# Performance work log

Hardware: AMD Instinct MI355X
Metric: run time of the kernel (lower is better)

The kernel has to match this reference:

```python
import jax, jax.numpy as jnp
import numpy as np


def setup_inputs() -> dict:
    key = jax.random.key(0)
    k1, _ = jax.random.split(key)
    N, H, CH, T = 4, 8, 64, 2048
    qkv = jax.random.normal(k1, (N, H * 3 * CH, T), dtype=jnp.float32)
    rescale = jnp.ones((1,), dtype=jnp.float32)
    return {"qkv": qkv, "rescale": rescale, "n_heads": H}


def reference(qkv, rescale, n_heads):
    bs, width, length = qkv.shape
    ch = width // (3 * n_heads)
    # [N, H*3*C, T] -> [N*H, 3*C, T] -> three [N*H, C, T]
    qkv_h = qkv.reshape(bs * n_heads, 3 * ch, length)
    q, k, v = qkv_h[:, :ch], qkv_h[:, ch:2 * ch], qkv_h[:, 2 * ch:]
    scale = 1.0 / jnp.sqrt(jnp.sqrt(jnp.float32(ch)))
    # scores: [B*H, T, S]
    weight = jnp.einsum('bct,bcs->bts', q * scale, k * scale)
    weight = jax.nn.softmax(weight.astype(jnp.float32) * rescale[0], axis=-1).astype(qkv.dtype)
    a = jnp.einsum('bts,bcs->bct', weight, v)  # [B*H, C, T]
    return a.reshape(bs, n_heads * ch, length)
```

## Files before the change

### kernel.cpp

```cpp
#include <hip/hip_runtime.h>
#include <stdint.h>

typedef _Float16 half8 __attribute__((ext_vector_type(8)));
typedef _Float16 half4 __attribute__((ext_vector_type(4)));
typedef __fp16   fp16x2 __attribute__((ext_vector_type(2)));
typedef float    floatx4 __attribute__((ext_vector_type(4)));

#define T_LEN 2048
#define CH 64
#define BH 32
#define QTILE 128
#define LDP 72
#define PTP 72
#define FRAG_BH 131072

__global__ __launch_bounds__(256, 2)
void prep_kernel(const float* __restrict__ qkv, const float* __restrict__ rescale,
                 _Float16* __restrict__ ws)
{
    __shared__ _Float16 Qs[64][LDP];
    __shared__ _Float16 Ks[64][LDP];
    __shared__ _Float16 Vs[64][LDP];

    const int tid  = threadIdx.x;
    const int bh   = blockIdx.y;
    const int tile = blockIdx.x;
    const int x0   = tile * 64;

    const float qscale = 0.125f * 1.4426950408889634f * rescale[0];

    const float* qp = qkv + (size_t)(bh >> 3) * (1536 * T_LEN)
                          + (size_t)(bh & 7) * (192 * T_LEN);
    const float* kp = qp + 64 * T_LEN;
    const float* vp = qp + 128 * T_LEN;

    {
        const int a4 = (tid & 15) * 4;
        const int c4 = (tid >> 4) * 4;
        float4 rq[4], rk[4];
#pragma unroll
        for (int i = 0; i < 4; ++i) {
            rq[i] = *(const float4*)(qp + (size_t)(c4 + i) * T_LEN + x0 + a4);
            rk[i] = *(const float4*)(kp + (size_t)(c4 + i) * T_LEN + x0 + a4);
        }
#pragma unroll
        for (int j = 0; j < 4; ++j) {
            half4 hq, hk;
#pragma unroll
            for (int i = 0; i < 4; ++i) {
                hq[i] = (_Float16)((&rq[i].x)[j] * qscale);
                hk[i] = (_Float16)((&rk[i].x)[j]);
            }
            *(half4*)&Qs[a4 + j][c4] = hq;
            *(half4*)&Ks[a4 + j][c4] = hk;
        }
        const int s4 = (tid & 15) * 4;
        const int cv = tid >> 4;
#pragma unroll
        for (int i = 0; i < 4; ++i) {
            const int c = cv + 16 * i;
            float4 r = *(const float4*)(vp + (size_t)c * T_LEN + x0 + s4);
            half4 h; h[0]=(_Float16)r.x; h[1]=(_Float16)r.y; h[2]=(_Float16)r.z; h[3]=(_Float16)r.w;
            *(half4*)&Vs[c][s4] = h;
        }
    }
    __syncthreads();

    const int lane = tid & 63, wave = tid >> 6;
    const int l15 = lane & 15, quad = lane >> 4;
    _Float16* qf = ws;
    _Float16* kf = ws + (size_t)BH * FRAG_BH;
    _Float16* vf = ws + (size_t)2 * BH * FRAG_BH;

#pragma unroll
    for (int ks = 0; ks < 2; ++ks) {
        half8 hq = *(const half8*)&Qs[wave * 16 + l15][ks * 32 + quad * 8];
        half8 hk = *(const half8*)&Ks[wave * 16 + l15][ks * 32 + quad * 8];
        half8 hv = *(const half8*)&Vs[wave * 16 + l15][ks * 32 + quad * 8];
        const size_t gqk = (((size_t)bh * 128 + tile * 4 + wave) * 2 + ks) * 512 + lane * 8;
        *(half8*)(qf + gqk) = hq;
        *(half8*)(kf + gqk) = hk;
        *(half8*)(vf + (((size_t)bh * 32 + tile) * 8 + wave * 2 + ks) * 512 + lane * 8) = hv;
    }
}

__global__ __launch_bounds__(256, 2)
void attn_kernel(const _Float16* __restrict__ ws, float* __restrict__ out)
{
    __shared__ _Float16 Pt[4][32][PTP];

    const int tid  = threadIdx.x;
    const int wave = tid >> 6;
    const int lane = tid & 63;
    const int l15  = lane & 15;
    const int quad = lane >> 4;

    const int bh = blockIdx.y;
    const int t0 = blockIdx.x * QTILE;

    const _Float16* qf = ws;
    const _Float16* kf = ws + (size_t)BH * FRAG_BH;
    const _Float16* vf = ws + (size_t)2 * BH * FRAG_BH;
    float* op = out + (size_t)bh * (CH * T_LEN);

    const _Float16* kfp = kf + (size_t)bh * FRAG_BH + lane * 8;
    const _Float16* vfp = vf + (size_t)bh * FRAG_BH + lane * 8;

    half8 bq[2][2];
#pragma unroll
    for (int tb = 0; tb < 2; ++tb)
#pragma unroll
        for (int ks = 0; ks < 2; ++ks)
            bq[tb][ks] = *(const half8*)(qf +
                (((size_t)bh * 128 + blockIdx.x * 8 + wave * 2 + tb) * 2 + ks) * 512 + lane * 8);

    const floatx4 fzero = {0.f, 0.f, 0.f, 0.f};
    floatx4 oacc[2][4];
#pragma unroll
    for (int tb = 0; tb < 2; ++tb)
#pragma unroll
        for (int ct = 0; ct < 4; ++ct) oacc[tb][ct] = fzero;
    floatx4 lacc[2] = {fzero, fzero};

    half8 bones;
#pragma unroll
    for (int i = 0; i < 8; ++i) bones[i] = (_Float16)1.0f;

    half8 ak[4][2];
    half8 bv[4][2];
    half8 ap[2][2];

    auto do_qk_exp = [&]() {
        floatx4 sacc[4][2];
#pragma unroll
        for (int mt = 0; mt < 4; ++mt)
#pragma unroll
            for (int tb = 0; tb < 2; ++tb) sacc[mt][tb] = fzero;
#pragma unroll
        for (int mt = 0; mt < 4; ++mt)
#pragma unroll
            for (int tb = 0; tb < 2; ++tb)
#pragma unroll
                for (int ks = 0; ks < 2; ++ks)
                    sacc[mt][tb] = __builtin_amdgcn_mfma_f32_16x16x32_f16(
                        ak[mt][ks], bq[tb][ks], sacc[mt][tb], 0, 0, 0);

#pragma unroll
        for (int mt = 0; mt < 4; ++mt)
#pragma unroll
            for (int tb = 0; tb < 2; ++tb) {
                fp16x2 p01 = __builtin_amdgcn_cvt_pkrtz(
                    __builtin_amdgcn_exp2f(sacc[mt][tb][0]),
                    __builtin_amdgcn_exp2f(sacc[mt][tb][1]));
                fp16x2 p23 = __builtin_amdgcn_cvt_pkrtz(
                    __builtin_amdgcn_exp2f(sacc[mt][tb][2]),
                    __builtin_amdgcn_exp2f(sacc[mt][tb][3]));
                half4 ph;
                ph[0] = (_Float16)p01[0]; ph[1] = (_Float16)p01[1];
                ph[2] = (_Float16)p23[0]; ph[3] = (_Float16)p23[1];
                *(half4*)&Pt[wave][tb * 16 + l15][mt * 16 + quad * 4] = ph;
            }
#pragma unroll
        for (int tb = 0; tb < 2; ++tb)
#pragma unroll
            for (int ks = 0; ks < 2; ++ks)
                ap[tb][ks] = *(const half8*)&Pt[wave][tb * 16 + l15][ks * 32 + quad * 8];
    };

#pragma unroll
    for (int mt = 0; mt < 4; ++mt)
#pragma unroll
        for (int ks = 0; ks < 2; ++ks)
            ak[mt][ks] = *(const half8*)(kfp + (size_t)(mt * 2 + ks) * 512);
#pragma unroll
    for (int ct = 0; ct < 4; ++ct)
#pragma unroll
        for (int ks = 0; ks < 2; ++ks)
            bv[ct][ks] = *(const half8*)(vfp + (size_t)(ct * 2 + ks) * 512);
    do_qk_exp();
#pragma unroll
    for (int mt = 0; mt < 4; ++mt)
#pragma unroll
        for (int ks = 0; ks < 2; ++ks)
            ak[mt][ks] = *(const half8*)(kfp + 4096 + (size_t)(mt * 2 + ks) * 512);

#pragma unroll 2
    for (int st = 1; st < 32; ++st) {
#pragma unroll
        for (int tb = 0; tb < 2; ++tb)
#pragma unroll
            for (int ks = 0; ks < 2; ++ks)
                lacc[tb] = __builtin_amdgcn_mfma_f32_16x16x32_f16(ap[tb][ks], bones, lacc[tb], 0, 0, 0);
#pragma unroll
        for (int tb = 0; tb < 2; ++tb)
#pragma unroll
            for (int ct = 0; ct < 4; ++ct)
#pragma unroll
                for (int ks = 0; ks < 2; ++ks)
                    oacc[tb][ct] = __builtin_amdgcn_mfma_f32_16x16x32_f16(
                        ap[tb][ks], bv[ct][ks], oacc[tb][ct], 0, 0, 0);

        const _Float16* vcur = vfp + (size_t)st * 4096;
#pragma unroll
        for (int ct = 0; ct < 4; ++ct)
#pragma unroll
            for (int ks = 0; ks < 2; ++ks)
                bv[ct][ks] = *(const half8*)(vcur + (size_t)(ct * 2 + ks) * 512);

        do_qk_exp();

        if (st < 31) {
            const _Float16* kcur = kfp + (size_t)(st + 1) * 4096;
#pragma unroll
            for (int mt = 0; mt < 4; ++mt)
#pragma unroll
                for (int ks = 0; ks < 2; ++ks)
                    ak[mt][ks] = *(const half8*)(kcur + (size_t)(mt * 2 + ks) * 512);
        }
    }

#pragma unroll
    for (int tb = 0; tb < 2; ++tb)
#pragma unroll
        for (int ks = 0; ks < 2; ++ks)
            lacc[tb] = __builtin_amdgcn_mfma_f32_16x16x32_f16(ap[tb][ks], bones, lacc[tb], 0, 0, 0);
#pragma unroll
    for (int tb = 0; tb < 2; ++tb)
#pragma unroll
        for (int ct = 0; ct < 4; ++ct)
#pragma unroll
            for (int ks = 0; ks < 2; ++ks)
                oacc[tb][ct] = __builtin_amdgcn_mfma_f32_16x16x32_f16(
                    ap[tb][ks], bv[ct][ks], oacc[tb][ct], 0, 0, 0);

#pragma unroll
    for (int tb = 0; tb < 2; ++tb) {
        float linv[4];
#pragma unroll
        for (int r = 0; r < 4; ++r) linv[r] = 1.0f / lacc[tb][r];
#pragma unroll
        for (int ct = 0; ct < 4; ++ct) {
            const int c = ct * 16 + l15;
            const int t = t0 + wave * 32 + tb * 16 + quad * 4;
            float4 o;
#pragma unroll
            for (int r = 0; r < 4; ++r)
                (&o.x)[r] = oacc[tb][ct][r] * linv[r];
            *(float4*)(op + (size_t)c * T_LEN + t) = o;
        }
    }
}

extern "C" void kernel_launch(void* const* d_in, const int* in_sizes, int n_in,
                              void* d_out, int out_size, void* d_ws, size_t ws_size,
                              hipStream_t stream) {
    const float* qkv     = (const float*)d_in[0];
    const float* rescale = (const float*)d_in[1];
    float* out = (float*)d_out;
    _Float16* ws = (_Float16*)d_ws;

    prep_kernel<<<dim3(32, BH), dim3(256), 0, stream>>>(qkv, rescale, ws);
    attn_kernel<<<dim3(T_LEN / QTILE, BH), dim3(256), 0, stream>>>(ws, out);
}
```

Baseline: 135.9 us.

## Replace LDS transpose of P with permlane swaps and XCD-aware block mapping

Converts the exponentiated score fragments from the MFMA accumulator layout into the A-operand layout using permlane32/permlane16 swap instructions in registers, instead of writing and reading them through a shared-memory buffer. This removes LDS stores and loads plus the shared allocation from the inner loop. The grid also becomes 1-D with a remapping that places all query tiles of a given head on the same XCD, so K/V fragments are more likely to be reused from that XCD's L2. The swap pattern has to match the exact lane layout, otherwise the output is silently wrong.

```diff
diff --git a/kernel.cpp b/kernel.cpp
--- a/kernel.cpp
+++ b/kernel.cpp
@@ -5,13 +5,14 @@
 typedef _Float16 half4 __attribute__((ext_vector_type(4)));
 typedef __fp16   fp16x2 __attribute__((ext_vector_type(2)));
 typedef float    floatx4 __attribute__((ext_vector_type(4)));
+typedef unsigned uintx2 __attribute__((ext_vector_type(2)));
+typedef unsigned uintx4 __attribute__((ext_vector_type(4)));
 
 #define T_LEN 2048
 #define CH 64
 #define BH 32
 #define QTILE 128
 #define LDP 72
-#define PTP 72
 #define FRAG_BH 131072
 
 __global__ __launch_bounds__(256, 2)
@@ -87,16 +88,18 @@
 __global__ __launch_bounds__(256, 2)
 void attn_kernel(const _Float16* __restrict__ ws, float* __restrict__ out)
 {
-    __shared__ _Float16 Pt[4][32][PTP];
-
     const int tid  = threadIdx.x;
     const int wave = tid >> 6;
     const int lane = tid & 63;
     const int l15  = lane & 15;
     const int quad = lane >> 4;
 
-    const int bh = blockIdx.y;
-    const int t0 = blockIdx.x * QTILE;
+    const int bid  = blockIdx.x;
+    const int xcd  = bid & 7;
+    const int slot = bid >> 3;
+    const int bh   = (slot >> 4) * 8 + xcd;
+    const int tile = slot & 15;
+    const int t0   = tile * QTILE;
 
     const _Float16* qf = ws;
     const _Float16* kf = ws + (size_t)BH * FRAG_BH;
@@ -112,7 +115,7 @@
 #pragma unroll
         for (int ks = 0; ks < 2; ++ks)
             bq[tb][ks] = *(const half8*)(qf +
-                (((size_t)bh * 128 + blockIdx.x * 8 + wave * 2 + tb) * 2 + ks) * 512 + lane * 8);
+                (((size_t)bh * 128 + tile * 8 + wave * 2 + tb) * 2 + ks) * 512 + lane * 8);
 
     const floatx4 fzero = {0.f, 0.f, 0.f, 0.f};
     floatx4 oacc[2][4];
@@ -146,25 +149,39 @@
                         ak[mt][ks], bq[tb][ks], sacc[mt][tb], 0, 0, 0);
 
 #pragma unroll
-        for (int mt = 0; mt < 4; ++mt)
-#pragma unroll
-            for (int tb = 0; tb < 2; ++tb) {
+        for (int tb = 0; tb < 2; ++tb) {
+            unsigned w[4][2];
+#pragma unroll
+            for (int mt = 0; mt < 4; ++mt) {
                 fp16x2 p01 = __builtin_amdgcn_cvt_pkrtz(
                     __builtin_amdgcn_exp2f(sacc[mt][tb][0]),
                     __builtin_amdgcn_exp2f(sacc[mt][tb][1]));
                 fp16x2 p23 = __builtin_amdgcn_cvt_pkrtz(
                     __builtin_amdgcn_exp2f(sacc[mt][tb][2]),
                     __builtin_amdgcn_exp2f(sacc[mt][tb][3]));
-                half4 ph;
-                ph[0] = (_Float16)p01[0]; ph[1] = (_Float16)p01[1];
-                ph[2] = (_Float16)p23[0]; ph[3] = (_Float16)p23[1];
-                *(half4*)&Pt[wave][tb * 16 + l15][mt * 16 + quad * 4] = ph;
+                w[mt][0] = __builtin_bit_cast(unsigned, p01);
+                w[mt][1] = __builtin_bit_cast(unsigned, p23);
             }
 #pragma unroll
-        for (int tb = 0; tb < 2; ++tb)
-#pragma unroll
-            for (int ks = 0; ks < 2; ++ks)
-                ap[tb][ks] = *(const half8*)&Pt[wave][tb * 16 + l15][ks * 32 + quad * 8];
+            for (int ks = 0; ks < 2; ++ks) {
+                uintx4 uu;
+                {
+                    uintx2 s1 = __builtin_amdgcn_permlane32_swap(
+                        w[2 * ks][0], w[2 * ks + 1][0], false, false);
+                    uintx2 s2 = __builtin_amdgcn_permlane16_swap(
+                        s1[0], s1[1], false, false);
+                    uu[0] = s2[0]; uu[2] = s2[1];
+                }
+                {
+                    uintx2 s1 = __builtin_amdgcn_permlane32_swap(
+                        w[2 * ks][1], w[2 * ks + 1][1], false, false);
+                    uintx2 s2 = __builtin_amdgcn_permlane16_swap(
+                        s1[0], s1[1], false, false);
+                    uu[1] = s2[0]; uu[3] = s2[1];
+                }
+                ap[tb][ks] = __builtin_bit_cast(half8, uu);
+            }
+        }
     };
 
 #pragma unroll
@@ -260,5 +277,5 @@
     _Float16* ws = (_Float16*)d_ws;
 
     prep_kernel<<<dim3(32, BH), dim3(256), 0, stream>>>(qkv, rescale, ws);
-    attn_kernel<<<dim3(T_LEN / QTILE, BH), dim3(256), 0, stream>>>(ws, out);
+    attn_kernel<<<dim3(T_LEN / QTILE * BH), dim3(256), 0, stream>>>(ws, out);
 }
```

New measurement: 143.4 us. 1.06x slower.

## Halve query tile per block and remap blocks so each head stays on one XCD

Applied to the files above, without the earlier changes.

Each wave now handles 16 query rows instead of 32, so the grid doubles to 1024 blocks and launch bounds allow 4 blocks per CU. A 1D grid is decoded so that blocks for the same head land on the same XCD (bid & 7), which is meant to improve L2 reuse of that head's K/V fragments. The cost is that each K/V fragment load now feeds half as many MFMAs, raising global/L2 traffic per FLOP, in exchange for more occupancy and latency hiding.

```diff
diff --git a/kernel.cpp b/kernel.cpp
--- a/kernel.cpp
+++ b/kernel.cpp
@@ -9,7 +9,7 @@
 #define T_LEN 2048
 #define CH 64
 #define BH 32
-#define QTILE 128
+#define QTILE 64
 #define LDP 72
 #define PTP 72
 #define FRAG_BH 131072
@@ -84,10 +84,10 @@
     }
 }
 
-__global__ __launch_bounds__(256, 2)
+__global__ __launch_bounds__(256, 4)
 void attn_kernel(const _Float16* __restrict__ ws, float* __restrict__ out)
 {
-    __shared__ _Float16 Pt[4][32][PTP];
+    __shared__ _Float16 Pt[4][16][PTP];
 
     const int tid  = threadIdx.x;
     const int wave = tid >> 6;
@@ -95,8 +95,12 @@
     const int l15  = lane & 15;
     const int quad = lane >> 4;
 
-    const int bh = blockIdx.y;
-    const int t0 = blockIdx.x * QTILE;
+    const int bid  = blockIdx.x;
+    const int xcd  = bid & 7;
+    const int slot = bid >> 3;
+    const int bh   = (slot & 3) * 8 + xcd;
+    const int tile = slot >> 2;
+    const int t0   = tile * QTILE;
 
     const _Float16* qf = ws;
     const _Float16* kf = ws + (size_t)BH * FRAG_BH;
@@ -106,21 +110,17 @@
     const _Float16* kfp = kf + (size_t)bh * FRAG_BH + lane * 8;
     const _Float16* vfp = vf + (size_t)bh * FRAG_BH + lane * 8;
 
-    half8 bq[2][2];
-#pragma unroll
-    for (int tb = 0; tb < 2; ++tb)
-#pragma unroll
-        for (int ks = 0; ks < 2; ++ks)
-            bq[tb][ks] = *(const half8*)(qf +
-                (((size_t)bh * 128 + blockIdx.x * 8 + wave * 2 + tb) * 2 + ks) * 512 + lane * 8);
+    half8 bq[2];
+#pragma unroll
+    for (int ks = 0; ks < 2; ++ks)
+        bq[ks] = *(const half8*)(qf +
+            (((size_t)bh * 128 + tile * 4 + wave) * 2 + ks) * 512 + lane * 8);
 
     const floatx4 fzero = {0.f, 0.f, 0.f, 0.f};
-    floatx4 oacc[2][4];
-#pragma unroll
-    for (int tb = 0; tb < 2; ++tb)
-#pragma unroll
-        for (int ct = 0; ct < 4; ++ct) oacc[tb][ct] = fzero;
-    floatx4 lacc[2] = {fzero, fzero};
+    floatx4 oacc[4];
+#pragma unroll
+    for (int ct = 0; ct < 4; ++ct) oacc[ct] = fzero;
+    floatx4 lacc = fzero;
 
     half8 bones;
 #pragma unroll
@@ -128,43 +128,35 @@
 
     half8 ak[4][2];
     half8 bv[4][2];
-    half8 ap[2][2];
+    half8 ap[2];
 
     auto do_qk_exp = [&]() {
-        floatx4 sacc[4][2];
+        floatx4 sacc[4];
+#pragma unroll
+        for (int mt = 0; mt < 4; ++mt) sacc[mt] = fzero;
 #pragma unroll
         for (int mt = 0; mt < 4; ++mt)
 #pragma unroll
-            for (int tb = 0; tb < 2; ++tb) sacc[mt][tb] = fzero;
-#pragma unroll
-        for (int mt = 0; mt < 4; ++mt)
-#pragma unroll
-            for (int tb = 0; tb < 2; ++tb)
-#pragma unroll
-                for (int ks = 0; ks < 2; ++ks)
-                    sacc[mt][tb] = __builtin_amdgcn_mfma_f32_16x16x32_f16(
-                        ak[mt][ks], bq[tb][ks], sacc[mt][tb], 0, 0, 0);
-
-#pragma unroll
-        for (int mt = 0; mt < 4; ++mt)
-#pragma unroll
-            for (int tb = 0; tb < 2; ++tb) {
-                fp16x2 p01 = __builtin_amdgcn_cvt_pkrtz(
-                    __builtin_amdgcn_exp2f(sacc[mt][tb][0]),
-                    __builtin_amdgcn_exp2f(sacc[mt][tb][1]));
-                fp16x2 p23 = __builtin_amdgcn_cvt_pkrtz(
-                    __builtin_amdgcn_exp2f(sacc[mt][tb][2]),
-                    __builtin_amdgcn_exp2f(sacc[mt][tb][3]));
-                half4 ph;
-                ph[0] = (_Float16)p01[0]; ph[1] = (_Float16)p01[1];
-                ph[2] = (_Float16)p23[0]; ph[3] = (_Float16)p23[1];
-                *(half4*)&Pt[wave][tb * 16 + l15][mt * 16 + quad * 4] = ph;
-            }
-#pragma unroll
-        for (int tb = 0; tb < 2; ++tb)
-#pragma unroll
             for (int ks = 0; ks < 2; ++ks)
-                ap[tb][ks] = *(const half8*)&Pt[wave][tb * 16 + l15][ks * 32 + quad * 8];
+                sacc[mt] = __builtin_amdgcn_mfma_f32_16x16x32_f16(
+                    ak[mt][ks], bq[ks], sacc[mt], 0, 0, 0);
+
+#pragma unroll
+        for (int mt = 0; mt < 4; ++mt) {
+            fp16x2 p01 = __builtin_amdgcn_cvt_pkrtz(
+                __builtin_amdgcn_exp2f(sacc[mt][0]),
+                __builtin_amdgcn_exp2f(sacc[mt][1]));
+            fp16x2 p23 = __builtin_amdgcn_cvt_pkrtz(
+                __builtin_amdgcn_exp2f(sacc[mt][2]),
+                __builtin_amdgcn_exp2f(sacc[mt][3]));
+            half4 ph;
+            ph[0] = (_Float16)p01[0]; ph[1] = (_Float16)p01[1];
+            ph[2] = (_Float16)p23[0]; ph[3] = (_Float16)p23[1];
+            *(half4*)&Pt[wave][l15][mt * 16 + quad * 4] = ph;
+        }
+#pragma unroll
+        for (int ks = 0; ks < 2; ++ks)
+            ap[ks] = *(const half8*)&Pt[wave][l15][ks * 32 + quad * 8];
     };
 
 #pragma unroll
@@ -187,18 +179,14 @@
 #pragma unroll 2
     for (int st = 1; st < 32; ++st) {
 #pragma unroll
-        for (int tb = 0; tb < 2; ++tb)
+        for (int ks = 0; ks < 2; ++ks)
+            lacc = __builtin_amdgcn_mfma_f32_16x16x32_f16(ap[ks], bones, lacc, 0, 0, 0);
+#pragma unroll
+        for (int ct = 0; ct < 4; ++ct)
 #pragma unroll
             for (int ks = 0; ks < 2; ++ks)
-                lacc[tb] = __builtin_amdgcn_mfma_f32_16x16x32_f16(ap[tb][ks], bones, lacc[tb], 0, 0, 0);
-#pragma unroll
-        for (int tb = 0; tb < 2; ++tb)
-#pragma unroll
-            for (int ct = 0; ct < 4; ++ct)
-#pragma unroll
-                for (int ks = 0; ks < 2; ++ks)
-                    oacc[tb][ct] = __builtin_amdgcn_mfma_f32_16x16x32_f16(
-                        ap[tb][ks], bv[ct][ks], oacc[tb][ct], 0, 0, 0);
+                oacc[ct] = __builtin_amdgcn_mfma_f32_16x16x32_f16(
+                    ap[ks], bv[ct][ks], oacc[ct], 0, 0, 0);
 
         const _Float16* vcur = vfp + (size_t)st * 4096;
 #pragma unroll
@@ -220,32 +208,27 @@
     }
 
 #pragma unroll
-    for (int tb = 0; tb < 2; ++tb)
-#pragma unroll
-        for (int ks = 0; ks < 2; ++ks)
-            lacc[tb] = __builtin_amdgcn_mfma_f32_16x16x32_f16(ap[tb][ks], bones, lacc[tb], 0, 0, 0);
-#pragma unroll
-    for (int tb = 0; tb < 2; ++tb)
-#pragma unroll
-        for (int ct = 0; ct < 4; ++ct)
-#pragma unroll
-            for (int ks = 0; ks < 2; ++ks)
-                oacc[tb][ct] = __builtin_amdgcn_mfma_f32_16x16x32_f16(
-                    ap[tb][ks], bv[ct][ks], oacc[tb][ct], 0, 0, 0);
-
-#pragma unroll
-    for (int tb = 0; tb < 2; ++tb) {
+    for (int ks = 0; ks < 2; ++ks)
+        lacc = __builtin_amdgcn_mfma_f32_16x16x32_f16(ap[ks], bones, lacc, 0, 0, 0);
+#pragma unroll
+    for (int ct = 0; ct < 4; ++ct)
+#pragma unroll
+        for (int ks = 0; ks < 2; ++ks)
+            oacc[ct] = __builtin_amdgcn_mfma_f32_16x16x32_f16(
+                ap[ks], bv[ct][ks], oacc[ct], 0, 0, 0);
+
+    {
         float linv[4];
 #pragma unroll
-        for (int r = 0; r < 4; ++r) linv[r] = 1.0f / lacc[tb][r];
+        for (int r = 0; r < 4; ++r) linv[r] = 1.0f / lacc[r];
 #pragma unroll
         for (int ct = 0; ct < 4; ++ct) {
             const int c = ct * 16 + l15;
-            const int t = t0 + wave * 32 + tb * 16 + quad * 4;
+            const int t = t0 + wave * 16 + quad * 4;
             float4 o;
 #pragma unroll
             for (int r = 0; r < 4; ++r)
-                (&o.x)[r] = oacc[tb][ct][r] * linv[r];
+                (&o.x)[r] = oacc[ct][r] * linv[r];
             *(float4*)(op + (size_t)c * T_LEN + t) = o;
         }
     }
@@ -260,5 +243,5 @@
     _Float16* ws = (_Float16*)d_ws;
 
     prep_kernel<<<dim3(32, BH), dim3(256), 0, stream>>>(qkv, rescale, ws);
-    attn_kernel<<<dim3(T_LEN / QTILE, BH), dim3(256), 0, stream>>>(ws, out);
+    attn_kernel<<<dim3(T_LEN / QTILE * BH), dim3(256), 0, stream>>>(ws, out);
 }
```

After: 153.5 us. 1.13x slower.

## Stage K/V tiles through LDS with async global_load_lds double buffering and XCD-aware block mapping

Applied to the files above, without the earlier changes.

Before, each wave loaded the full K and V fragments straight from global memory into registers, so every wave fetched the same data. Now the block cooperatively loads each K/V step into double-buffered LDS using async global-to-LDS loads, and waves read their fragments from LDS. This cuts redundant global traffic fourfold and lets the next step's load overlap compute. The grid is also flattened with a remapping that puts all tiles of one head on the same XCD for L2 reuse. The cost is extra LDS, a __syncthreads per iteration, and more LDS read traffic.

```diff
diff --git a/kernel.cpp b/kernel.cpp
--- a/kernel.cpp
+++ b/kernel.cpp
@@ -84,9 +84,17 @@
     }
 }
 
+__device__ __forceinline__ void gload16(const _Float16* g, _Float16* l) {
+    __builtin_amdgcn_global_load_lds(
+        (const __attribute__((address_space(1))) void*)g,
+        (__attribute__((address_space(3))) void*)l, 16, 0, 0);
+}
+
 __global__ __launch_bounds__(256, 2)
 void attn_kernel(const _Float16* __restrict__ ws, float* __restrict__ out)
 {
+    __shared__ _Float16 Kb[2][4096];
+    __shared__ _Float16 Vb[2][4096];
     __shared__ _Float16 Pt[4][32][PTP];
 
     const int tid  = threadIdx.x;
@@ -95,16 +103,31 @@
     const int l15  = lane & 15;
     const int quad = lane >> 4;
 
-    const int bh = blockIdx.y;
-    const int t0 = blockIdx.x * QTILE;
+    const int bid  = blockIdx.x;
+    const int xcd  = bid & 7;
+    const int slot = bid >> 3;
+    const int bh   = (slot >> 4) * 8 + xcd;
+    const int tile = slot & 15;
+    const int t0   = tile * QTILE;
 
     const _Float16* qf = ws;
     const _Float16* kf = ws + (size_t)BH * FRAG_BH;
     const _Float16* vf = ws + (size_t)2 * BH * FRAG_BH;
     float* op = out + (size_t)bh * (CH * T_LEN);
 
-    const _Float16* kfp = kf + (size_t)bh * FRAG_BH + lane * 8;
-    const _Float16* vfp = vf + (size_t)bh * FRAG_BH + lane * 8;
+    const _Float16* ktile = kf + (size_t)bh * FRAG_BH;
+    const _Float16* vtile = vf + (size_t)bh * FRAG_BH;
+
+    auto stage = [&](int st, int buf) {
+        const _Float16* kg = ktile + (size_t)st * 4096 + wave * 1024 + lane * 8;
+        const _Float16* vg = vtile + (size_t)st * 4096 + wave * 1024 + lane * 8;
+        _Float16* kl = &Kb[buf][wave * 1024];
+        _Float16* vl = &Vb[buf][wave * 1024];
+        gload16(kg,       kl);
+        gload16(kg + 512, kl + 512);
+        gload16(vg,       vl);
+        gload16(vg + 512, vl + 512);
+    };
 
     half8 bq[2][2];
 #pragma unroll
@@ -112,7 +135,7 @@
 #pragma unroll
         for (int ks = 0; ks < 2; ++ks)
             bq[tb][ks] = *(const half8*)(qf +
-                (((size_t)bh * 128 + blockIdx.x * 8 + wave * 2 + tb) * 2 + ks) * 512 + lane * 8);
+                (((size_t)bh * 128 + tile * 8 + wave * 2 + tb) * 2 + ks) * 512 + lane * 8);
 
     const floatx4 fzero = {0.f, 0.f, 0.f, 0.f};
     floatx4 oacc[2][4];
@@ -129,6 +152,21 @@
     half8 ak[4][2];
     half8 bv[4][2];
     half8 ap[2][2];
+
+    auto read_ak = [&](int buf) {
+#pragma unroll
+        for (int mt = 0; mt < 4; ++mt)
+#pragma unroll
+            for (int ks = 0; ks < 2; ++ks)
+                ak[mt][ks] = *(const half8*)&Kb[buf][(mt * 2 + ks) * 512 + lane * 8];
+    };
+    auto read_bv = [&](int buf) {
+#pragma unroll
+        for (int ct = 0; ct < 4; ++ct)
+#pragma unroll
+            for (int ks = 0; ks < 2; ++ks)
+                bv[ct][ks] = *(const half8*)&Vb[buf][(ct * 2 + ks) * 512 + lane * 8];
+    };
 
     auto do_qk_exp = [&]() {
         floatx4 sacc[4][2];
@@ -167,25 +205,19 @@
                 ap[tb][ks] = *(const half8*)&Pt[wave][tb * 16 + l15][ks * 32 + quad * 8];
     };
 
-#pragma unroll
-    for (int mt = 0; mt < 4; ++mt)
-#pragma unroll
-        for (int ks = 0; ks < 2; ++ks)
-            ak[mt][ks] = *(const half8*)(kfp + (size_t)(mt * 2 + ks) * 512);
-#pragma unroll
-    for (int ct = 0; ct < 4; ++ct)
-#pragma unroll
-        for (int ks = 0; ks < 2; ++ks)
-            bv[ct][ks] = *(const half8*)(vfp + (size_t)(ct * 2 + ks) * 512);
+    stage(0, 0);
+    __syncthreads();
+    read_ak(0);
+    read_bv(0);
+    stage(1, 1);
     do_qk_exp();
-#pragma unroll
-    for (int mt = 0; mt < 4; ++mt)
-#pragma unroll
-        for (int ks = 0; ks < 2; ++ks)
-            ak[mt][ks] = *(const half8*)(kfp + 4096 + (size_t)(mt * 2 + ks) * 512);
-
-#pragma unroll 2
+    __syncthreads();
+    read_ak(1);
+
     for (int st = 1; st < 32; ++st) {
+        const int cur = st & 1;
+        if (st < 31) stage(st + 1, cur ^ 1);
+
 #pragma unroll
         for (int tb = 0; tb < 2; ++tb)
 #pragma unroll
@@ -200,23 +232,12 @@
                     oacc[tb][ct] = __builtin_amdgcn_mfma_f32_16x16x32_f16(
                         ap[tb][ks], bv[ct][ks], oacc[tb][ct], 0, 0, 0);
 
-        const _Float16* vcur = vfp + (size_t)st * 4096;
-#pragma unroll
-        for (int ct = 0; ct < 4; ++ct)
-#pragma unroll
-            for (int ks = 0; ks < 2; ++ks)
-                bv[ct][ks] = *(const half8*)(vcur + (size_t)(ct * 2 + ks) * 512);
-
         do_qk_exp();
 
-        if (st < 31) {
-            const _Float16* kcur = kfp + (size_t)(st + 1) * 4096;
-#pragma unroll
-            for (int mt = 0; mt < 4; ++mt)
-#pragma unroll
-                for (int ks = 0; ks < 2; ++ks)
-                    ak[mt][ks] = *(const half8*)(kcur + (size_t)(mt * 2 + ks) * 512);
-        }
+        read_bv(cur);
+
+        __syncthreads();
+        if (st < 31) read_ak(cur ^ 1);
     }
 
 #pragma unroll
@@ -260,5 +281,5 @@
     _Float16* ws = (_Float16*)d_ws;
 
     prep_kernel<<<dim3(32, BH), dim3(256), 0, stream>>>(qkv, rescale, ws);
-    attn_kernel<<<dim3(T_LEN / QTILE, BH), dim3(256), 0, stream>>>(ws, out);
-}
+    attn_kernel<<<dim3(T_LEN / QTILE * BH), dim3(256), 0, stream>>>(ws, out);
+}
```

Result: faster. 132.3 us (-2.6%).
